# Kernel optimization log

Hardware: AMD Instinct MI355X
Metric: run time of the kernel (lower is better)

## Reference

```python
import jax, jax.numpy as jnp
import numpy as np

DIM, K_RANK, L, N_CLASS = 64, 16, 8, 10
H = 1e-3
B = 256
DD = DIM * DIM  # 4096


def _cay(C, D):
    # Cayley transform of B = C @ D^T : I + C (I - 0.5 D^T C)^{-1} D^T
    Id = jnp.eye(C.shape[1], dtype=C.dtype)
    DT = jnp.swapaxes(D, 1, 2)
    inv = jnp.linalg.inv(Id - 0.5 * DT @ C)
    return Id + C @ inv @ DT


def setup_inputs() -> dict:
    key = jax.random.key(0)
    ks = jax.random.split(key, 9)
    u = jax.random.normal(ks[0], (B, DIM, K_RANK), jnp.float32) / np.float32(np.sqrt(DIM))
    vh = jax.random.normal(ks[1], (B, K_RANK, DIM), jnp.float32) / np.float32(np.sqrt(DIM))
    eye_k = jnp.eye(K_RANK, dtype=jnp.float32)
    off = 0.05 * jax.random.normal(ks[2], (B, K_RANK, K_RANK), jnp.float32) * (1.0 - eye_k)
    dvals = jax.random.uniform(ks[3], (B, K_RANK), jnp.float32, 0.5, 1.5)
    s_core = off + dvals[:, :, None] * eye_k  # diag bounded away from 0 (invert_S)
    s_block = jnp.zeros((B, DIM, K_RANK), jnp.float32).at[:, :K_RANK, :K_RANK].set(s_core)
    X = jnp.stack([u.reshape(B, -1), s_block.reshape(B, -1), vh.reshape(B, -1)], axis=1)
    sc = np.float32(1.0 / np.sqrt(DD))
    W0 = sc * jax.random.normal(ks[4], (DD, DD), jnp.float32)
    W = sc * jax.random.normal(ks[5], (L, DD, DD), jnp.float32)
    b = sc * jax.random.normal(ks[6], (L, DD), jnp.float32)
    Wc = sc * jax.random.normal(ks[7], (N_CLASS, DD), jnp.float32)
    bc = sc * jax.random.normal(ks[8], (N_CLASS,), jnp.float32)
    return {"X": X, "W0": W0, "W": W, "b": b, "Wc": Wc, "bc": bc}


def reference(X, W0, W, b, Wc, bc):
    Bn = X.shape[0]
    u = X[:, 0].reshape(Bn, DIM, K_RANK)
    s = X[:, 1].reshape(Bn, DIM, K_RANK)[:, :K_RANK, :K_RANK]
    vh = X[:, 2].reshape(Bn, K_RANK, DIM)
    v = jnp.swapaxes(vh, 1, 2)
    eye_k = jnp.eye(K_RANK, dtype=X.dtype)
    eye_d = jnp.eye(DIM, dtype=X.dtype)
    Xf = (u @ s @ vh).reshape(Bn, DD)
    outs = []
    for i in range(L + 1):  # layer 0 has no bias
        lin = Xf @ W0.T if i == 0 else Xf @ W[i - 1].T + b[i - 1]
        dY = jax.nn.relu(lin).reshape(Bn, DIM, DIM)
        # invert_S: invert only the diagonal of s
        s_inv = (1.0 / jnp.diagonal(s, axis1=1, axis2=2))[:, :, None] * eye_k
        dU = dY @ v @ s_inv
        dV = jnp.swapaxes(dY, 1, 2) @ u @ jnp.swapaxes(s_inv, 1, 2)
        dS = jnp.swapaxes(u, 1, 2) @ dY @ v
        uT = jnp.swapaxes(u, 1, 2)
        F = (eye_d - u @ uT) @ dU
        FT = jnp.swapaxes(F, 1, 2)
        u = _cay(H * (F @ uT), -H * (u @ FT)) @ u
        vT = jnp.swapaxes(v, 1, 2)
        F = (eye_d - v @ vT) @ dV
        FT = jnp.swapaxes(F, 1, 2)
        v = _cay(H * (F @ vT), -H * (v @ FT)) @ v
        s = s + H * dS
        Xf = (u @ s @ jnp.swapaxes(v, 1, 2)).reshape(Bn, DD)
        outs.append(Xf)
    X_transformed = jnp.stack(outs, axis=-1)  # (B, dim*dim, L+1)
    X_classified = Xf @ Wc.T + bc
    X_predicted = jax.nn.softmax(X_classified, axis=1)
    return X_predicted, X_classified, X_transformed
```

## Files before the change

### kernel.cpp

```cpp
#include <hip/hip_runtime.h>
#include <hip/hip_cooperative_groups.h>
#include <math.h>

namespace cg = cooperative_groups;

typedef unsigned short u16;
typedef unsigned int u32;
using bf16x8 = __attribute__((ext_vector_type(8))) short;
using f32x4  = __attribute__((ext_vector_type(4))) float;

#define DD 4096
#define NB 256
#define SPLIT_K 8
#define PSTRIDE (NB * DD)
#define PLANE (NB * DD)

__device__ __forceinline__ u16 f2bf(float f) {
  unsigned int u = __float_as_uint(f);
  u += 0x7fffu + ((u >> 16) & 1u);
  return (u16)(u >> 16);
}
__device__ __forceinline__ float bf2f(u16 h) {
  return __uint_as_float((u32)h << 16);
}
__device__ __forceinline__ unsigned int pack2bf(float a, float b) {
  return (unsigned int)f2bf(a) | ((unsigned int)f2bf(b) << 16);
}
__device__ __forceinline__ void async_cp16(const u16* g, u16* l) {
  __builtin_amdgcn_global_load_lds(
      (const __attribute__((address_space(1))) unsigned int*)g,
      (__attribute__((address_space(3))) unsigned int*)l, 16, 0, 0);
}

struct GemmSmem {
  u16 As[256 * 64];
  u16 Bs[64 * 64];
};
struct UpdSmem {
  float U[64][17], V[64][17], P[64][17], Q[64][17];
  float S[16][16];
  float sinv[16];
  union {
    float dY[64][68];
    struct {
      float F[64][17];
      float T1[16][17], G1[16][17], G2[16][17], M1[16][17], dSs[16][17];
      float RS[512];
    };
  };
};
struct PackSmem { float buf[512 * 9]; };
struct ClsSmem  { float red[8][10]; };

__device__ __forceinline__ void gemm_phase(
    GemmSmem& sm, const u16* __restrict__ A, const float* __restrict__ W,
    u16* __restrict__ part, int tile, int t)
{
  const int nt = tile & 63, kz = tile >> 6;
  const int w = t >> 6, l = t & 63;
  const int colg0 = nt << 6;
  const int k0 = kz << 9;

  f32x4 acc[4][2];
#pragma unroll
  for (int mi = 0; mi < 4; ++mi)
#pragma unroll
    for (int nj = 0; nj < 2; ++nj)
      acc[mi][nj] = (f32x4){0.f, 0.f, 0.f, 0.f};

  const int wm = w & 3, wn = w >> 2;
  const int lr = l & 15, lg = l >> 4;
  const int arow_l = (w << 3) + (l >> 3);
  const int acl = l & 7;
  const int bn_l = t >> 3;
  const int bcc = t & 7;

  for (int tt = 0; tt < 8; ++tt) {
    const int kk = k0 + (tt << 6);
    __syncthreads();
#pragma unroll
    for (int r = 0; r < 4; ++r) {
      const int row = (r << 6) + arow_l;
      const int cs = acl ^ (row & 7);
      async_cp16(A + ((size_t)row << 12) + kk + (cs << 3),
                 &sm.As[(r << 12) + (w << 9)]);
    }
    {
      const float* wsrc = W + ((size_t)(colg0 + bn_l) << 12) + kk + (bcc << 3);
      const float4 f0 = *reinterpret_cast<const float4*>(wsrc);
      const float4 f1 = *reinterpret_cast<const float4*>(wsrc + 4);
      uint4 pk;
      pk.x = pack2bf(f0.x, f0.y);
      pk.y = pack2bf(f0.z, f0.w);
      pk.z = pack2bf(f1.x, f1.y);
      pk.w = pack2bf(f1.z, f1.w);
      *reinterpret_cast<uint4*>(&sm.Bs[(bn_l << 6) + ((bcc ^ (bn_l & 7)) << 3)]) = pk;
    }
    __syncthreads();
#pragma unroll
    for (int ks = 0; ks < 2; ++ks) {
      const int cg2 = (ks << 2) + lg;
      bf16x8 av[4], bv[2];
#pragma unroll
      for (int mi = 0; mi < 4; ++mi) {
        const int fr = (wm << 6) + (mi << 4) + lr;
        av[mi] = *reinterpret_cast<const bf16x8*>(&sm.As[(fr << 6) + ((cg2 ^ (fr & 7)) << 3)]);
      }
#pragma unroll
      for (int nj = 0; nj < 2; ++nj) {
        const int fc = (wn << 5) + (nj << 4) + lr;
        bv[nj] = *reinterpret_cast<const bf16x8*>(&sm.Bs[(fc << 6) + ((cg2 ^ (fc & 7)) << 3)]);
      }
#pragma unroll
      for (int mi = 0; mi < 4; ++mi)
#pragma unroll
        for (int nj = 0; nj < 2; ++nj)
          acc[mi][nj] = __builtin_amdgcn_mfma_f32_16x16x32_bf16(
              av[mi], bv[nj], acc[mi][nj], 0, 0, 0);
    }
  }

  u16* pout = part + (size_t)kz * PSTRIDE;
#pragma unroll
  for (int mi = 0; mi < 4; ++mi)
#pragma unroll
    for (int nj = 0; nj < 2; ++nj) {
      const int col = colg0 + (wn << 5) + (nj << 4) + lr;
#pragma unroll
      for (int j = 0; j < 4; ++j) {
        const int row = (wm << 6) + (mi << 4) + (lg << 2) + j;
        pout[((size_t)row << 12) + col] = f2bf(acc[mi][nj][j]);
      }
    }
}

__device__ __forceinline__ void stiefel_update512(
    UpdSmem& m, float (&Am)[64][17], float (&Dm)[64][17],
    int t, float* __restrict__ gout, size_t ub)
{
  const int p = t >> 3;
  const int j0 = (t << 1) & 15;
  {
    const int half = t & 1, i = t >> 5, j = (t >> 1) & 15;
    float a = 0.f;
    const int r0 = half << 5;
    for (int r = r0; r < r0 + 32; ++r) a += Am[r][i] * Dm[r][j];
    m.RS[t] = a;
  }
  __syncthreads();
  if (t < 256) m.T1[t >> 4][t & 15] = m.RS[t << 1] + m.RS[(t << 1) + 1];
  __syncthreads();
  {
    float f0 = Dm[p][j0], f1 = Dm[p][j0 + 1];
    for (int k = 0; k < 16; ++k) {
      const float ak = Am[p][k];
      f0 -= ak * m.T1[k][j0];
      f1 -= ak * m.T1[k][j0 + 1];
    }
    m.F[p][j0] = f0; m.F[p][j0 + 1] = f1;
  }
  __syncthreads();
  if (t < 256) {
    const int i = t >> 4, j = t & 15;
    float g = 0.f;
    for (int r = 0; r < 64; ++r) g += Am[r][i] * m.F[r][j];
    m.G1[i][j] = g;
  } else {
    const int tt = t - 256, i = tt >> 4, j = tt & 15;
    float g = 0.f;
    for (int r = 0; r < 64; ++r) g += Am[r][i] * Am[r][j];
    m.G2[i][j] = g;
  }
  __syncthreads();
  if (t < 256) {
    const int i = t >> 4, j = t & 15;
    float mm = 0.f;
    for (int k = 0; k < 16; ++k) mm += m.G1[i][k] * m.G2[k][j];
    m.M1[i][j] = mm;
  }
  __syncthreads();
  {
    float a0 = 0.f, a1 = 0.f;
    for (int k = 0; k < 16; ++k) {
      const float fk = m.F[p][k];
      a0 += fk * m.M1[k][j0];
      a1 += fk * m.M1[k][j0 + 1];
    }
    const float n0 = Am[p][j0] - 1e-6f * a0;
    const float n1 = Am[p][j0 + 1] - 1e-6f * a1;
    __syncthreads();
    Am[p][j0] = n0; Am[p][j0 + 1] = n1;
    *reinterpret_cast<float2*>(gout + ub + (p << 4) + j0) = make_float2(n0, n1);
  }
  __syncthreads();
}

__device__ __forceinline__ void write_xf_tail(
    UpdSmem& m, int t, int b, float* __restrict__ Xf, u16* __restrict__ Xfb,
    float* __restrict__ outL_plane)
{
  const int p = t >> 3;
  const int j0 = (t << 1) & 15;
  {
    float a0 = 0.f, a1 = 0.f;
    for (int k = 0; k < 16; ++k) {
      const float uk = m.U[p][k];
      a0 += uk * m.S[k][j0];
      a1 += uk * m.S[k][j0 + 1];
    }
    m.P[p][j0] = a0; m.P[p][j0 + 1] = a1;
  }
  __syncthreads();
  {
    const int q0 = (t & 7) << 3;
    float res[8];
#pragma unroll
    for (int e = 0; e < 8; ++e) res[e] = 0.f;
    for (int i = 0; i < 16; ++i) {
      const float pi = m.P[p][i];
#pragma unroll
      for (int e = 0; e < 8; ++e) res[e] += pi * m.V[q0 + e][i];
    }
    const size_t ko = ((size_t)b << 12) + (p << 6) + q0;
    float4* xo = reinterpret_cast<float4*>(Xf + ko);
    const float4 r0 = make_float4(res[0], res[1], res[2], res[3]);
    const float4 r1 = make_float4(res[4], res[5], res[6], res[7]);
    xo[0] = r0; xo[1] = r1;
    uint4 pk;
    pk.x = pack2bf(res[0], res[1]); pk.y = pack2bf(res[2], res[3]);
    pk.z = pack2bf(res[4], res[5]); pk.w = pack2bf(res[6], res[7]);
    *reinterpret_cast<uint4*>(Xfb + ko) = pk;
    if (outL_plane != nullptr) {
      float4* op = reinterpret_cast<float4*>(outL_plane + ko);
      op[0] = r0; op[1] = r1;
    }
  }
}

__device__ __forceinline__ void update_phase(
    UpdSmem& m, const u16* __restrict__ part, const float* __restrict__ bias,
    float* __restrict__ u_g, float* __restrict__ v_g, float* __restrict__ s_g,
    float* __restrict__ Xf, u16* __restrict__ Xfb,
    float* __restrict__ outL_plane, int b, int t)
{
  const size_t ub = (size_t)b << 10;
  {
    const float2 u2 = *reinterpret_cast<const float2*>(u_g + ub + (t << 1));
    const float2 v2 = *reinterpret_cast<const float2*>(v_g + ub + (t << 1));
    const int r = t >> 3, c = (t & 7) << 1;
    m.U[r][c] = u2.x; m.U[r][c + 1] = u2.y;
    m.V[r][c] = v2.x; m.V[r][c + 1] = v2.y;
    if (t < 256) m.S[t >> 4][t & 15] = s_g[((size_t)b << 8) + t];
  }
  __syncthreads();
  if (t < 16) m.sinv[t] = 1.0f / m.S[t][t];
  {
    const u16* p0 = part + ((size_t)b << 12) + (t << 3);
    float x[8];
#pragma unroll
    for (int e = 0; e < 8; ++e) x[e] = 0.f;
#pragma unroll
    for (int kzi = 0; kzi < SPLIT_K; ++kzi) {
      const uint4 v = *reinterpret_cast<const uint4*>(p0 + (size_t)kzi * PSTRIDE);
      x[0] += bf2f((u16)(v.x & 0xffff)); x[1] += bf2f((u16)(v.x >> 16));
      x[2] += bf2f((u16)(v.y & 0xffff)); x[3] += bf2f((u16)(v.y >> 16));
      x[4] += bf2f((u16)(v.z & 0xffff)); x[5] += bf2f((u16)(v.z >> 16));
      x[6] += bf2f((u16)(v.w & 0xffff)); x[7] += bf2f((u16)(v.w >> 16));
    }
    if (bias != nullptr) {
      const float4 b0 = *reinterpret_cast<const float4*>(bias + (t << 3));
      const float4 b1 = *reinterpret_cast<const float4*>(bias + (t << 3) + 4);
      x[0] += b0.x; x[1] += b0.y; x[2] += b0.z; x[3] += b0.w;
      x[4] += b1.x; x[5] += b1.y; x[6] += b1.z; x[7] += b1.w;
    }
    const int r = t >> 3, c = (t & 7) << 3;
    float4* d0 = reinterpret_cast<float4*>(&m.dY[r][c]);
    d0[0] = make_float4(fmaxf(x[0], 0.f), fmaxf(x[1], 0.f), fmaxf(x[2], 0.f), fmaxf(x[3], 0.f));
    d0[1] = make_float4(fmaxf(x[4], 0.f), fmaxf(x[5], 0.f), fmaxf(x[6], 0.f), fmaxf(x[7], 0.f));
  }
  __syncthreads();
  const int p = t >> 3;
  const int j0 = (t << 1) & 15;
  {
    float a0 = 0.f, a1 = 0.f;
    for (int q = 0; q < 64; ++q) {
      const float d = m.dY[p][q];
      a0 += d * m.V[q][j0];
      a1 += d * m.V[q][j0 + 1];
    }
    float b0 = 0.f, b1 = 0.f;
    for (int r = 0; r < 64; ++r) {
      const float d = m.dY[r][p];
      b0 += d * m.U[r][j0];
      b1 += d * m.U[r][j0 + 1];
    }
    m.P[p][j0] = a0; m.P[p][j0 + 1] = a1;
    m.Q[p][j0] = b0; m.Q[p][j0 + 1] = b1;
  }
  __syncthreads();
  {
    const int half = t & 1, i = t >> 5, j = (t >> 1) & 15;
    float a = 0.f;
    const int r0 = half << 5;
    for (int r = r0; r < r0 + 32; ++r) a += m.U[r][i] * m.P[r][j];
    m.RS[t] = a;
  }
  __syncthreads();
  if (t < 256) m.dSs[t >> 4][t & 15] = m.RS[t << 1] + m.RS[(t << 1) + 1];
  __syncthreads();
  for (int i = t; i < 1024; i += 512) {
    const int r = i >> 4, c = i & 15;
    const float sc = m.sinv[c];
    m.P[r][c] *= sc;
    m.Q[r][c] *= sc;
  }
  __syncthreads();

  stiefel_update512(m, m.U, m.P, t, u_g, ub);
  stiefel_update512(m, m.V, m.Q, t, v_g, ub);

  if (t < 256) {
    const int i = t >> 4, j = t & 15;
    const float ns = m.S[i][j] + 1e-3f * m.dSs[i][j];
    m.S[i][j] = ns;
    s_g[((size_t)b << 8) + t] = ns;
  }
  __syncthreads();
  write_xf_tail(m, t, b, Xf, Xfb, outL_plane);
}

__device__ __forceinline__ void init_phase(
    UpdSmem& m, const float* __restrict__ X,
    float* __restrict__ u_g, float* __restrict__ v_g, float* __restrict__ s_g,
    float* __restrict__ Xf, u16* __restrict__ Xfb, int b, int t)
{
  const float* xb = X + (size_t)b * 3072;
  const size_t ub = (size_t)b << 10;
  {
    const float2 u2 = *reinterpret_cast<const float2*>(xb + (t << 1));
    const int r = t >> 3, c = (t & 7) << 1;
    m.U[r][c] = u2.x; m.U[r][c + 1] = u2.y;
    *reinterpret_cast<float2*>(u_g + ub + (t << 1)) = u2;
    if (t < 256) {
      const float sv = xb[1024 + t];
      m.S[t >> 4][t & 15] = sv;
      s_g[((size_t)b << 8) + t] = sv;
    }
    const float2 v2 = *reinterpret_cast<const float2*>(xb + 2048 + (t << 1));
    const int g2 = t << 1;
    const int iv = g2 >> 6, q = g2 & 63;
    m.V[q][iv] = v2.x; m.V[q + 1][iv] = v2.y;
    v_g[ub + (size_t)q * 16 + iv] = v2.x;
    v_g[ub + (size_t)(q + 1) * 16 + iv] = v2.y;
  }
  __syncthreads();
  write_xf_tail(m, t, b, Xf, Xfb, nullptr);
}

__global__ __launch_bounds__(512, 4) void mega_kernel(
    const float* __restrict__ X, const float* __restrict__ W0,
    const float* __restrict__ W, const float* __restrict__ bb,
    const float* __restrict__ Wc, const float* __restrict__ bc,
    float* __restrict__ pred, float* __restrict__ cls, float* __restrict__ outT,
    float* __restrict__ Xf, u16* __restrict__ part,
    float* __restrict__ u_g, float* __restrict__ v_g, float* __restrict__ s_g,
    u16* __restrict__ Xfb, float* __restrict__ outL)
{
  cg::grid_group grid = cg::this_grid();
  __shared__ __align__(16) char smem_raw[sizeof(GemmSmem)];
  GemmSmem& gs = *reinterpret_cast<GemmSmem*>(smem_raw);
  UpdSmem&  us = *reinterpret_cast<UpdSmem*>(smem_raw);
  PackSmem& ps = *reinterpret_cast<PackSmem*>(smem_raw);
  ClsSmem&  cs = *reinterpret_cast<ClsSmem*>(smem_raw);

  const int g = blockIdx.x, t = threadIdx.x;
  const int nwg = gridDim.x;

  for (int b = g; b < NB; b += nwg)
    init_phase(us, X, u_g, v_g, s_g, Xf, Xfb, b, t);
  grid.sync();

  for (int layer = 0; layer <= 8; ++layer) {
    const float* Wl = (layer == 0) ? W0 : W + (size_t)(layer - 1) * DD * DD;
    for (int tile = g; tile < 64 * SPLIT_K; tile += nwg)
      gemm_phase(gs, Xfb, Wl, part, tile, t);
    grid.sync();
    for (int b = g; b < NB; b += nwg)
      update_phase(us, part, (layer == 0) ? nullptr : (bb + (size_t)(layer - 1) * DD),
                   u_g, v_g, s_g, Xf, Xfb,
                   outL + (size_t)layer * PLANE, b, t);
    grid.sync();
  }

  for (int b = g; b < NB; b += nwg) {
    const int lane = t & 63, w = t >> 6;
    float acc[10];
#pragma unroll
    for (int c = 0; c < 10; ++c) acc[c] = 0.f;
    const float* xr = Xf + ((size_t)b << 12);
    for (int k = t; k < 4096; k += 512) {
      const float x = xr[k];
#pragma unroll
      for (int c = 0; c < 10; ++c) acc[c] += x * Wc[c * 4096 + k];
    }
#pragma unroll
    for (int c = 0; c < 10; ++c)
      for (int off = 32; off; off >>= 1) acc[c] += __shfl_xor(acc[c], off);
    if (lane == 0)
#pragma unroll
      for (int c = 0; c < 10; ++c) cs.red[w][c] = acc[c];
    __syncthreads();
    if (t == 0) {
      float lg[10], ex[10];
      float mx = -1e30f;
#pragma unroll
      for (int c = 0; c < 10; ++c) {
        float s8 = 0.f;
#pragma unroll
        for (int ww = 0; ww < 8; ++ww) s8 += cs.red[ww][c];
        lg[c] = s8 + bc[c];
        mx = fmaxf(mx, lg[c]);
      }
      float s = 0.f;
#pragma unroll
      for (int c = 0; c < 10; ++c) { ex[c] = expf(lg[c] - mx); s += ex[c]; }
      const float inv = 1.f / s;
#pragma unroll
      for (int c = 0; c < 10; ++c) {
        cls[b * 10 + c] = lg[c];
        pred[b * 10 + c] = ex[c] * inv;
      }
    }
    __syncthreads();
  }

  for (int ch = g; ch < 2048; ch += nwg) {
    const int base = ch << 9;
#pragma unroll
    for (int l = 0; l < 9; ++l)
      ps.buf[t * 9 + l] = outL[(size_t)l * PLANE + base + t];
    __syncthreads();
    const float4* b4 = reinterpret_cast<const float4*>(ps.buf);
    float4* o4 = reinterpret_cast<float4*>(outT + (size_t)base * 9);
    for (int i = t; i < 1152; i += 512) o4[i] = b4[i];
    __syncthreads();
  }
}

__global__ __launch_bounds__(512, 4) void gemm_kernel(
    const u16* __restrict__ A, const float* __restrict__ W,
    u16* __restrict__ part)
{
  __shared__ __align__(16) GemmSmem sm;
  gemm_phase(sm, A, W, part, (int)(blockIdx.x + (blockIdx.y << 6)), (int)threadIdx.x);
}

__global__ __launch_bounds__(512) void update_kernel(
    const u16* __restrict__ part, const float* __restrict__ bias,
    float* __restrict__ u_g, float* __restrict__ v_g, float* __restrict__ s_g,
    float* __restrict__ Xf, u16* __restrict__ Xfb,
    float* __restrict__ outL, int layer)
{
  __shared__ __align__(16) UpdSmem m;
  update_phase(m, part, bias, u_g, v_g, s_g, Xf, Xfb,
               outL + (size_t)layer * PLANE, (int)blockIdx.x, (int)threadIdx.x);
}

__global__ __launch_bounds__(512) void init_kernel(
    const float* __restrict__ X, float* __restrict__ u_g, float* __restrict__ v_g,
    float* __restrict__ s_g, float* __restrict__ Xf, u16* __restrict__ Xfb)
{
  __shared__ __align__(16) UpdSmem m;
  init_phase(m, X, u_g, v_g, s_g, Xf, Xfb, (int)blockIdx.x, (int)threadIdx.x);
}

__global__ __launch_bounds__(256) void pack_kernel(
    const float* __restrict__ outL, float* __restrict__ outT)
{
  const int t = threadIdx.x;
  const int base = blockIdx.x << 8;
  __shared__ float buf[256 * 9];
#pragma unroll
  for (int l = 0; l < 9; ++l)
    buf[t * 9 + l] = outL[(size_t)l * PLANE + base + t];
  __syncthreads();
  const float4* b4 = reinterpret_cast<const float4*>(buf);
  float4* o4 = reinterpret_cast<float4*>(outT + (size_t)base * 9);
  for (int i = t; i < 576; i += 256) o4[i] = b4[i];
}

__global__ __launch_bounds__(256) void classifier_kernel(
    const float* __restrict__ Xf, const float* __restrict__ Wc,
    const float* __restrict__ bc, float* __restrict__ pred, float* __restrict__ cls)
{
  const int b = blockIdx.x, t = threadIdx.x;
  const int lane = t & 63, w = t >> 6;
  __shared__ float red[4][10];
  float acc[10];
#pragma unroll
  for (int c = 0; c < 10; ++c) acc[c] = 0.f;
  const float* xr = Xf + ((size_t)b << 12);
  for (int k = t; k < 4096; k += 256) {
    const float x = xr[k];
#pragma unroll
    for (int c = 0; c < 10; ++c) acc[c] += x * Wc[c * 4096 + k];
  }
#pragma unroll
  for (int c = 0; c < 10; ++c)
    for (int off = 32; off; off >>= 1) acc[c] += __shfl_xor(acc[c], off);
  if (lane == 0)
#pragma unroll
    for (int c = 0; c < 10; ++c) red[w][c] = acc[c];
  __syncthreads();
  if (t == 0) {
    float lg[10], ex[10];
    float m = -1e30f;
#pragma unroll
    for (int c = 0; c < 10; ++c) {
      lg[c] = red[0][c] + red[1][c] + red[2][c] + red[3][c] + bc[c];
      m = fmaxf(m, lg[c]);
    }
    float s = 0.f;
#pragma unroll
    for (int c = 0; c < 10; ++c) { ex[c] = expf(lg[c] - m); s += ex[c]; }
    const float inv = 1.f / s;
#pragma unroll
    for (int c = 0; c < 10; ++c) {
      cls[b * 10 + c] = lg[c];
      pred[b * 10 + c] = ex[c] * inv;
    }
  }
}

extern "C" void kernel_launch(void* const* d_in, const int* in_sizes, int n_in,
                              void* d_out, int out_size, void* d_ws, size_t ws_size,
                              hipStream_t stream) {
  (void)in_sizes; (void)n_in; (void)out_size; (void)ws_size;
  const float* X  = (const float*)d_in[0];
  const float* W0 = (const float*)d_in[1];
  const float* W  = (const float*)d_in[2];
  const float* bb = (const float*)d_in[3];
  const float* Wc = (const float*)d_in[4];
  const float* bc = (const float*)d_in[5];

  float* out_pred  = (float*)d_out;
  float* out_cls   = out_pred + 2560;
  float* out_trans = out_pred + 5120;

  char* ws = (char*)d_ws;
  float* Xf   = (float*)(ws);
  u16*   part = (u16*)  (ws + (4ull << 20));
  float* u_g  = (float*)(ws + (20ull << 20));
  float* v_g  = (float*)(ws + (21ull << 20));
  float* s_g  = (float*)(ws + (22ull << 20));
  u16*   Xfb  = (u16*)  (ws + (23ull << 20));
  float* outL = (float*)(ws + (25ull << 20));

  int occ = 0;
  (void)hipOccupancyMaxActiveBlocksPerMultiprocessor(
      &occ, (const void*)mega_kernel, 512, 0);

  bool done = false;
  if (occ >= 2) {
    void* kargs[] = {
      (void*)&X, (void*)&W0, (void*)&W, (void*)&bb, (void*)&Wc, (void*)&bc,
      (void*)&out_pred, (void*)&out_cls, (void*)&out_trans,
      (void*)&Xf, (void*)&part, (void*)&u_g, (void*)&v_g, (void*)&s_g,
      (void*)&Xfb, (void*)&outL
    };
    hipError_t e = hipLaunchCooperativeKernel((const void*)mega_kernel,
                                              dim3(512), dim3(512),
                                              kargs, 0, stream);
    if (e == hipSuccess) done = true;
    else (void)hipGetLastError();
  }

  if (!done) {
    init_kernel<<<NB, 512, 0, stream>>>(X, u_g, v_g, s_g, Xf, Xfb);
    for (int i = 0; i <= 8; ++i) {
      const float* Wl = (i == 0) ? W0 : W + (size_t)(i - 1) * DD * DD;
      gemm_kernel<<<dim3(64, SPLIT_K), 512, 0, stream>>>(Xfb, Wl, part);
      update_kernel<<<NB, 512, 0, stream>>>(
          part, (i == 0) ? nullptr : (bb + (size_t)(i - 1) * DD),
          u_g, v_g, s_g, Xf, Xfb, outL, i);
    }
    pack_kernel<<<4096, 256, 0, stream>>>(outL, out_trans);
    classifier_kernel<<<NB, 256, 0, stream>>>(Xf, Wc, bc, out_pred, out_cls);
  }
}
```

Baseline: 436.5 us.

## Double-buffer GEMM LDS tiles and prefetch next K-slice during MFMA

```diff
diff --git a/kernel.cpp b/kernel.cpp
--- a/kernel.cpp
+++ b/kernel.cpp
@@ -33,8 +33,8 @@
 }
 
 struct GemmSmem {
-  u16 As[256 * 64];
-  u16 Bs[64 * 64];
+  u16 As[2][256 * 64];
+  u16 Bs[2][64 * 64];
 };
 struct UpdSmem {
   float U[64][17], V[64][17], P[64][17], Q[64][17];
@@ -75,28 +75,47 @@
   const int bn_l = t >> 3;
   const int bcc = t & 7;
 
+  float4 b0[2], b1[2];
+
+#define ISSUE_A(tt) do {                                                     \
+    const int kkk = k0 + ((tt) << 6);                                        \
+    _Pragma("unroll")                                                        \
+    for (int r = 0; r < 4; ++r) {                                            \
+      const int row = (r << 6) + arow_l;                                     \
+      const int cs = acl ^ (row & 7);                                        \
+      async_cp16(A + ((size_t)row << 12) + kkk + (cs << 3),                  \
+                 &sm.As[(tt) & 1][(r << 12) + (w << 9)]);                    \
+    } } while (0)
+
+#define LOAD_B(tt) do {                                                      \
+    const float* wsrc = W + ((size_t)(colg0 + bn_l) << 12) + k0 +            \
+                        ((tt) << 6) + (bcc << 3);                            \
+    b0[(tt) & 1] = *reinterpret_cast<const float4*>(wsrc);                   \
+    b1[(tt) & 1] = *reinterpret_cast<const float4*>(wsrc + 4);               \
+  } while (0)
+
+  ISSUE_A(0); LOAD_B(0);
+  __builtin_amdgcn_sched_barrier(0);
+
+#pragma unroll
   for (int tt = 0; tt < 8; ++tt) {
-    const int kk = k0 + (tt << 6);
-    __syncthreads();
-#pragma unroll
-    for (int r = 0; r < 4; ++r) {
-      const int row = (r << 6) + arow_l;
-      const int cs = acl ^ (row & 7);
-      async_cp16(A + ((size_t)row << 12) + kk + (cs << 3),
-                 &sm.As[(r << 12) + (w << 9)]);
-    }
+    const int pb = tt & 1;
+    if (tt < 7) { ISSUE_A(tt + 1); LOAD_B(tt + 1); }
+    __builtin_amdgcn_sched_barrier(0);
+    if (tt < 7) { asm volatile("s_waitcnt vmcnt(6)" ::: "memory"); }
+    else        { asm volatile("s_waitcnt vmcnt(0)" ::: "memory"); }
+    __builtin_amdgcn_sched_barrier(0);
     {
-      const float* wsrc = W + ((size_t)(colg0 + bn_l) << 12) + kk + (bcc << 3);
-      const float4 f0 = *reinterpret_cast<const float4*>(wsrc);
-      const float4 f1 = *reinterpret_cast<const float4*>(wsrc + 4);
       uint4 pk;
-      pk.x = pack2bf(f0.x, f0.y);
-      pk.y = pack2bf(f0.z, f0.w);
-      pk.z = pack2bf(f1.x, f1.y);
-      pk.w = pack2bf(f1.z, f1.w);
-      *reinterpret_cast<uint4*>(&sm.Bs[(bn_l << 6) + ((bcc ^ (bn_l & 7)) << 3)]) = pk;
-    }
-    __syncthreads();
+      pk.x = pack2bf(b0[pb].x, b0[pb].y);
+      pk.y = pack2bf(b0[pb].z, b0[pb].w);
+      pk.z = pack2bf(b1[pb].x, b1[pb].y);
+      pk.w = pack2bf(b1[pb].z, b1[pb].w);
+      *reinterpret_cast<uint4*>(&sm.Bs[pb][(bn_l << 6) + ((bcc ^ (bn_l & 7)) << 3)]) = pk;
+    }
+    asm volatile("s_waitcnt lgkmcnt(0)" ::: "memory");
+    __builtin_amdgcn_s_barrier();
+    __builtin_amdgcn_sched_barrier(0);
 #pragma unroll
     for (int ks = 0; ks < 2; ++ks) {
       const int cg2 = (ks << 2) + lg;
@@ -104,12 +123,12 @@
 #pragma unroll
       for (int mi = 0; mi < 4; ++mi) {
         const int fr = (wm << 6) + (mi << 4) + lr;
-        av[mi] = *reinterpret_cast<const bf16x8*>(&sm.As[(fr << 6) + ((cg2 ^ (fr & 7)) << 3)]);
+        av[mi] = *reinterpret_cast<const bf16x8*>(&sm.As[pb][(fr << 6) + ((cg2 ^ (fr & 7)) << 3)]);
       }
 #pragma unroll
       for (int nj = 0; nj < 2; ++nj) {
         const int fc = (wn << 5) + (nj << 4) + lr;
-        bv[nj] = *reinterpret_cast<const bf16x8*>(&sm.Bs[(fc << 6) + ((cg2 ^ (fc & 7)) << 3)]);
+        bv[nj] = *reinterpret_cast<const bf16x8*>(&sm.Bs[pb][(fc << 6) + ((cg2 ^ (fc & 7)) << 3)]);
       }
 #pragma unroll
       for (int mi = 0; mi < 4; ++mi)
@@ -118,7 +137,10 @@
           acc[mi][nj] = __builtin_amdgcn_mfma_f32_16x16x32_bf16(
               av[mi], bv[nj], acc[mi][nj], 0, 0, 0);
     }
-  }
+    __builtin_amdgcn_s_barrier();
+  }
+#undef ISSUE_A
+#undef LOAD_B
 
   u16* pout = part + (size_t)kz * PSTRIDE;
 #pragma unroll
```

Measured after the change: 441.3 us. About the same (+1.1%).

## Replace cooperative mega-kernel with per-layer launches and double split-K

Applied to the files above, without the earlier changes.

```diff
diff --git a/kernel.cpp b/kernel.cpp
--- a/kernel.cpp
+++ b/kernel.cpp
@@ -1,8 +1,5 @@
 #include <hip/hip_runtime.h>
-#include <hip/hip_cooperative_groups.h>
 #include <math.h>
-
-namespace cg = cooperative_groups;
 
 typedef unsigned short u16;
 typedef unsigned int u32;
@@ -11,7 +8,7 @@
 
 #define DD 4096
 #define NB 256
-#define SPLIT_K 8
+#define SPLIT_K 16
 #define PSTRIDE (NB * DD)
 #define PLANE (NB * DD)
 
@@ -32,10 +29,94 @@
       (__attribute__((address_space(3))) unsigned int*)l, 16, 0, 0);
 }
 
-struct GemmSmem {
-  u16 As[256 * 64];
-  u16 Bs[64 * 64];
-};
+__global__ __launch_bounds__(512, 8) void gemm_kernel(
+    const u16* __restrict__ A, const float* __restrict__ W,
+    u16* __restrict__ part)
+{
+  const int nt = blockIdx.x;
+  const int kz = blockIdx.y;
+  const int t = threadIdx.x;
+  const int w = t >> 6, l = t & 63;
+
+  __shared__ __align__(16) u16 As[256 * 64];
+  __shared__ __align__(16) u16 Bs[64 * 64];
+
+  const int colg0 = nt << 6;
+  const int k0 = kz << 8;
+
+  f32x4 acc[4][2];
+#pragma unroll
+  for (int mi = 0; mi < 4; ++mi)
+#pragma unroll
+    for (int nj = 0; nj < 2; ++nj)
+      acc[mi][nj] = (f32x4){0.f, 0.f, 0.f, 0.f};
+
+  const int wm = w & 3, wn = w >> 2;
+  const int lr = l & 15, lg = l >> 4;
+  const int arow_l = (w << 3) + (l >> 3);
+  const int acl = l & 7;
+  const int bn_l = t >> 3;
+  const int bcc = t & 7;
+
+  for (int tt = 0; tt < 4; ++tt) {
+    const int kk = k0 + (tt << 6);
+    __syncthreads();
+#pragma unroll
+    for (int r = 0; r < 4; ++r) {
+      const int row = (r << 6) + arow_l;
+      const int cs = acl ^ (row & 7);
+      async_cp16(A + ((size_t)row << 12) + kk + (cs << 3),
+                 &As[(r << 12) + (w << 9)]);
+    }
+    {
+      const float* wsrc = W + ((size_t)(colg0 + bn_l) << 12) + kk + (bcc << 3);
+      const float4 f0 = *reinterpret_cast<const float4*>(wsrc);
+      const float4 f1 = *reinterpret_cast<const float4*>(wsrc + 4);
+      uint4 pk;
+      pk.x = pack2bf(f0.x, f0.y);
+      pk.y = pack2bf(f0.z, f0.w);
+      pk.z = pack2bf(f1.x, f1.y);
+      pk.w = pack2bf(f1.z, f1.w);
+      *reinterpret_cast<uint4*>(&Bs[(bn_l << 6) + ((bcc ^ (bn_l & 7)) << 3)]) = pk;
+    }
+    __syncthreads();
+#pragma unroll
+    for (int ks = 0; ks < 2; ++ks) {
+      const int cg = (ks << 2) + lg;
+      bf16x8 av[4], bv[2];
+#pragma unroll
+      for (int mi = 0; mi < 4; ++mi) {
+        const int fr = (wm << 6) + (mi << 4) + lr;
+        av[mi] = *reinterpret_cast<const bf16x8*>(&As[(fr << 6) + ((cg ^ (fr & 7)) << 3)]);
+      }
+#pragma unroll
+      for (int nj = 0; nj < 2; ++nj) {
+        const int fc = (wn << 5) + (nj << 4) + lr;
+        bv[nj] = *reinterpret_cast<const bf16x8*>(&Bs[(fc << 6) + ((cg ^ (fc & 7)) << 3)]);
+      }
+#pragma unroll
+      for (int mi = 0; mi < 4; ++mi)
+#pragma unroll
+        for (int nj = 0; nj < 2; ++nj)
+          acc[mi][nj] = __builtin_amdgcn_mfma_f32_16x16x32_bf16(
+              av[mi], bv[nj], acc[mi][nj], 0, 0, 0);
+    }
+  }
+
+  u16* pout = part + (size_t)kz * PSTRIDE;
+#pragma unroll
+  for (int mi = 0; mi < 4; ++mi)
+#pragma unroll
+    for (int nj = 0; nj < 2; ++nj) {
+      const int col = colg0 + (wn << 5) + (nj << 4) + lr;
+#pragma unroll
+      for (int j = 0; j < 4; ++j) {
+        const int row = (wm << 6) + (mi << 4) + (lg << 2) + j;
+        pout[((size_t)row << 12) + col] = f2bf(acc[mi][nj][j]);
+      }
+    }
+}
+
 struct UpdSmem {
   float U[64][17], V[64][17], P[64][17], Q[64][17];
   float S[16][16];
@@ -49,90 +130,6 @@
     };
   };
 };
-struct PackSmem { float buf[512 * 9]; };
-struct ClsSmem  { float red[8][10]; };
-
-__device__ __forceinline__ void gemm_phase(
-    GemmSmem& sm, const u16* __restrict__ A, const float* __restrict__ W,
-    u16* __restrict__ part, int tile, int t)
-{
-  const int nt = tile & 63, kz = tile >> 6;
-  const int w = t >> 6, l = t & 63;
-  const int colg0 = nt << 6;
-  const int k0 = kz << 9;
-
-  f32x4 acc[4][2];
-#pragma unroll
-  for (int mi = 0; mi < 4; ++mi)
-#pragma unroll
-    for (int nj = 0; nj < 2; ++nj)
-      acc[mi][nj] = (f32x4){0.f, 0.f, 0.f, 0.f};
-
-  const int wm = w & 3, wn = w >> 2;
-  const int lr = l & 15, lg = l >> 4;
-  const int arow_l = (w << 3) + (l >> 3);
-  const int acl = l & 7;
-  const int bn_l = t >> 3;
-  const int bcc = t & 7;
-
-  for (int tt = 0; tt < 8; ++tt) {
-    const int kk = k0 + (tt << 6);
-    __syncthreads();
-#pragma unroll
-    for (int r = 0; r < 4; ++r) {
-      const int row = (r << 6) + arow_l;
-      const int cs = acl ^ (row & 7);
-      async_cp16(A + ((size_t)row << 12) + kk + (cs << 3),
-                 &sm.As[(r << 12) + (w << 9)]);
-    }
-    {
-      const float* wsrc = W + ((size_t)(colg0 + bn_l) << 12) + kk + (bcc << 3);
-      const float4 f0 = *reinterpret_cast<const float4*>(wsrc);
-      const float4 f1 = *reinterpret_cast<const float4*>(wsrc + 4);
-      uint4 pk;
-      pk.x = pack2bf(f0.x, f0.y);
-      pk.y = pack2bf(f0.z, f0.w);
-      pk.z = pack2bf(f1.x, f1.y);
-      pk.w = pack2bf(f1.z, f1.w);
-      *reinterpret_cast<uint4*>(&sm.Bs[(bn_l << 6) + ((bcc ^ (bn_l & 7)) << 3)]) = pk;
-    }
-    __syncthreads();
-#pragma unroll
-    for (int ks = 0; ks < 2; ++ks) {
-      const int cg2 = (ks << 2) + lg;
-      bf16x8 av[4], bv[2];
-#pragma unroll
-      for (int mi = 0; mi < 4; ++mi) {
-        const int fr = (wm << 6) + (mi << 4) + lr;
-        av[mi] = *reinterpret_cast<const bf16x8*>(&sm.As[(fr << 6) + ((cg2 ^ (fr & 7)) << 3)]);
-      }
-#pragma unroll
-      for (int nj = 0; nj < 2; ++nj) {
-        const int fc = (wn << 5) + (nj << 4) + lr;
-        bv[nj] = *reinterpret_cast<const bf16x8*>(&sm.Bs[(fc << 6) + ((cg2 ^ (fc & 7)) << 3)]);
-      }
-#pragma unroll
-      for (int mi = 0; mi < 4; ++mi)
-#pragma unroll
-        for (int nj = 0; nj < 2; ++nj)
-          acc[mi][nj] = __builtin_amdgcn_mfma_f32_16x16x32_bf16(
-              av[mi], bv[nj], acc[mi][nj], 0, 0, 0);
-    }
-  }
-
-  u16* pout = part + (size_t)kz * PSTRIDE;
-#pragma unroll
-  for (int mi = 0; mi < 4; ++mi)
-#pragma unroll
-    for (int nj = 0; nj < 2; ++nj) {
-      const int col = colg0 + (wn << 5) + (nj << 4) + lr;
-#pragma unroll
-      for (int j = 0; j < 4; ++j) {
-        const int row = (wm << 6) + (mi << 4) + (lg << 2) + j;
-        pout[((size_t)row << 12) + col] = f2bf(acc[mi][nj][j]);
-      }
-    }
-}
 
 __device__ __forceinline__ void stiefel_update512(
     UpdSmem& m, float (&Am)[64][17], float (&Dm)[64][17],
@@ -237,12 +234,16 @@
   }
 }
 
-__device__ __forceinline__ void update_phase(
-    UpdSmem& m, const u16* __restrict__ part, const float* __restrict__ bias,
+__global__ __launch_bounds__(512) void update_kernel(
+    const u16* __restrict__ part, const float* __restrict__ bias,
     float* __restrict__ u_g, float* __restrict__ v_g, float* __restrict__ s_g,
     float* __restrict__ Xf, u16* __restrict__ Xfb,
-    float* __restrict__ outL_plane, int b, int t)
-{
+    float* __restrict__ outL, int layer)
+{
+  const int b = blockIdx.x, t = threadIdx.x;
+  __shared__ __align__(16) UpdSmem m;
+  float* outL_plane = outL + (size_t)layer * PLANE;
+
   const size_t ub = (size_t)b << 10;
   {
     const float2 u2 = *reinterpret_cast<const float2*>(u_g + ub + (t << 1));
@@ -329,11 +330,12 @@
   write_xf_tail(m, t, b, Xf, Xfb, outL_plane);
 }
 
-__device__ __forceinline__ void init_phase(
-    UpdSmem& m, const float* __restrict__ X,
-    float* __restrict__ u_g, float* __restrict__ v_g, float* __restrict__ s_g,
-    float* __restrict__ Xf, u16* __restrict__ Xfb, int b, int t)
-{
+__global__ __launch_bounds__(512) void init_kernel(
+    const float* __restrict__ X, float* __restrict__ u_g, float* __restrict__ v_g,
+    float* __restrict__ s_g, float* __restrict__ Xf, u16* __restrict__ Xfb)
+{
+  const int b = blockIdx.x, t = threadIdx.x;
+  __shared__ __align__(16) UpdSmem m;
   const float* xb = X + (size_t)b * 3072;
   const size_t ub = (size_t)b << 10;
   {
@@ -355,123 +357,6 @@
   }
   __syncthreads();
   write_xf_tail(m, t, b, Xf, Xfb, nullptr);
-}
-
-__global__ __launch_bounds__(512, 4) void mega_kernel(
-    const float* __restrict__ X, const float* __restrict__ W0,
-    const float* __restrict__ W, const float* __restrict__ bb,
-    const float* __restrict__ Wc, const float* __restrict__ bc,
-    float* __restrict__ pred, float* __restrict__ cls, float* __restrict__ outT,
-    float* __restrict__ Xf, u16* __restrict__ part,
-    float* __restrict__ u_g, float* __restrict__ v_g, float* __restrict__ s_g,
-    u16* __restrict__ Xfb, float* __restrict__ outL)
-{
-  cg::grid_group grid = cg::this_grid();
-  __shared__ __align__(16) char smem_raw[sizeof(GemmSmem)];
-  GemmSmem& gs = *reinterpret_cast<GemmSmem*>(smem_raw);
-  UpdSmem&  us = *reinterpret_cast<UpdSmem*>(smem_raw);
-  PackSmem& ps = *reinterpret_cast<PackSmem*>(smem_raw);
-  ClsSmem&  cs = *reinterpret_cast<ClsSmem*>(smem_raw);
-
-  const int g = blockIdx.x, t = threadIdx.x;
-  const int nwg = gridDim.x;
-
-  for (int b = g; b < NB; b += nwg)
-    init_phase(us, X, u_g, v_g, s_g, Xf, Xfb, b, t);
-  grid.sync();
-
-  for (int layer = 0; layer <= 8; ++layer) {
-    const float* Wl = (layer == 0) ? W0 : W + (size_t)(layer - 1) * DD * DD;
-    for (int tile = g; tile < 64 * SPLIT_K; tile += nwg)
-      gemm_phase(gs, Xfb, Wl, part, tile, t);
-    grid.sync();
-    for (int b = g; b < NB; b += nwg)
-      update_phase(us, part, (layer == 0) ? nullptr : (bb + (size_t)(layer - 1) * DD),
-                   u_g, v_g, s_g, Xf, Xfb,
-                   outL + (size_t)layer * PLANE, b, t);
-    grid.sync();
-  }
-
-  for (int b = g; b < NB; b += nwg) {
-    const int lane = t & 63, w = t >> 6;
-    float acc[10];
-#pragma unroll
-    for (int c = 0; c < 10; ++c) acc[c] = 0.f;
-    const float* xr = Xf + ((size_t)b << 12);
-    for (int k = t; k < 4096; k += 512) {
-      const float x = xr[k];
-#pragma unroll
-      for (int c = 0; c < 10; ++c) acc[c] += x * Wc[c * 4096 + k];
-    }
-#pragma unroll
-    for (int c = 0; c < 10; ++c)
-      for (int off = 32; off; off >>= 1) acc[c] += __shfl_xor(acc[c], off);
-    if (lane == 0)
-#pragma unroll
-      for (int c = 0; c < 10; ++c) cs.red[w][c] = acc[c];
-    __syncthreads();
-    if (t == 0) {
-      float lg[10], ex[10];
-      float mx = -1e30f;
-#pragma unroll
-      for (int c = 0; c < 10; ++c) {
-        float s8 = 0.f;
-#pragma unroll
-        for (int ww = 0; ww < 8; ++ww) s8 += cs.red[ww][c];
-        lg[c] = s8 + bc[c];
-        mx = fmaxf(mx, lg[c]);
-      }
-      float s = 0.f;
-#pragma unroll
-      for (int c = 0; c < 10; ++c) { ex[c] = expf(lg[c] - mx); s += ex[c]; }
-      const float inv = 1.f / s;
-#pragma unroll
-      for (int c = 0; c < 10; ++c) {
-        cls[b * 10 + c] = lg[c];
-        pred[b * 10 + c] = ex[c] * inv;
-      }
-    }
-    __syncthreads();
-  }
-
-  for (int ch = g; ch < 2048; ch += nwg) {
-    const int base = ch << 9;
-#pragma unroll
-    for (int l = 0; l < 9; ++l)
-      ps.buf[t * 9 + l] = outL[(size_t)l * PLANE + base + t];
-    __syncthreads();
-    const float4* b4 = reinterpret_cast<const float4*>(ps.buf);
-    float4* o4 = reinterpret_cast<float4*>(outT + (size_t)base * 9);
-    for (int i = t; i < 1152; i += 512) o4[i] = b4[i];
-    __syncthreads();
-  }
-}
-
-__global__ __launch_bounds__(512, 4) void gemm_kernel(
-    const u16* __restrict__ A, const float* __restrict__ W,
-    u16* __restrict__ part)
-{
-  __shared__ __align__(16) GemmSmem sm;
-  gemm_phase(sm, A, W, part, (int)(blockIdx.x + (blockIdx.y << 6)), (int)threadIdx.x);
-}
-
-__global__ __launch_bounds__(512) void update_kernel(
-    const u16* __restrict__ part, const float* __restrict__ bias,
-    float* __restrict__ u_g, float* __restrict__ v_g, float* __restrict__ s_g,
-    float* __restrict__ Xf, u16* __restrict__ Xfb,
-    float* __restrict__ outL, int layer)
-{
-  __shared__ __align__(16) UpdSmem m;
-  update_phase(m, part, bias, u_g, v_g, s_g, Xf, Xfb,
-               outL + (size_t)layer * PLANE, (int)blockIdx.x, (int)threadIdx.x);
-}
-
-__global__ __launch_bounds__(512) void init_kernel(
-    const float* __restrict__ X, float* __restrict__ u_g, float* __restrict__ v_g,
-    float* __restrict__ s_g, float* __restrict__ Xf, u16* __restrict__ Xfb)
-{
-  __shared__ __align__(16) UpdSmem m;
-  init_phase(m, X, u_g, v_g, s_g, Xf, Xfb, (int)blockIdx.x, (int)threadIdx.x);
 }
 
 __global__ __launch_bounds__(256) void pack_kernel(
@@ -550,41 +435,20 @@
   char* ws = (char*)d_ws;
   float* Xf   = (float*)(ws);
   u16*   part = (u16*)  (ws + (4ull << 20));
-  float* u_g  = (float*)(ws + (20ull << 20));
-  float* v_g  = (float*)(ws + (21ull << 20));
-  float* s_g  = (float*)(ws + (22ull << 20));
-  u16*   Xfb  = (u16*)  (ws + (23ull << 20));
-  float* outL = (float*)(ws + (25ull << 20));
-
-  int occ = 0;
-  (void)hipOccupancyMaxActiveBlocksPerMultiprocessor(
-      &occ, (const void*)mega_kernel, 512, 0);
-
-  bool done = false;
-  if (occ >= 2) {
-    void* kargs[] = {
-      (void*)&X, (void*)&W0, (void*)&W, (void*)&bb, (void*)&Wc, (void*)&bc,
-      (void*)&out_pred, (void*)&out_cls, (void*)&out_trans,
-      (void*)&Xf, (void*)&part, (void*)&u_g, (void*)&v_g, (void*)&s_g,
-      (void*)&Xfb, (void*)&outL
-    };
-    hipError_t e = hipLaunchCooperativeKernel((const void*)mega_kernel,
-                                              dim3(512), dim3(512),
-                                              kargs, 0, stream);
-    if (e == hipSuccess) done = true;
-    else (void)hipGetLastError();
-  }
-
-  if (!done) {
-    init_kernel<<<NB, 512, 0, stream>>>(X, u_g, v_g, s_g, Xf, Xfb);
-    for (int i = 0; i <= 8; ++i) {
-      const float* Wl = (i == 0) ? W0 : W + (size_t)(i - 1) * DD * DD;
-      gemm_kernel<<<dim3(64, SPLIT_K), 512, 0, stream>>>(Xfb, Wl, part);
-      update_kernel<<<NB, 512, 0, stream>>>(
-          part, (i == 0) ? nullptr : (bb + (size_t)(i - 1) * DD),
-          u_g, v_g, s_g, Xf, Xfb, outL, i);
-    }
-    pack_kernel<<<4096, 256, 0, stream>>>(outL, out_trans);
-    classifier_kernel<<<NB, 256, 0, stream>>>(Xf, Wc, bc, out_pred, out_cls);
-  }
-}
+  float* u_g  = (float*)(ws + (36ull << 20));
+  float* v_g  = (float*)(ws + (37ull << 20));
+  float* s_g  = (float*)(ws + (38ull << 20));
+  u16*   Xfb  = (u16*)  (ws + (39ull << 20));
+  float* outL = (float*)(ws + (41ull << 20));
+
+  init_kernel<<<NB, 512, 0, stream>>>(X, u_g, v_g, s_g, Xf, Xfb);
+  for (int i = 0; i <= 8; ++i) {
+    const float* Wl = (i == 0) ? W0 : W + (size_t)(i - 1) * DD * DD;
+    gemm_kernel<<<dim3(64, SPLIT_K), 512, 0, stream>>>(Xfb, Wl, part);
+    update_kernel<<<NB, 512, 0, stream>>>(
+        part, (i == 0) ? nullptr : (bb + (size_t)(i - 1) * DD),
+        u_g, v_g, s_g, Xf, Xfb, outL, i);
+  }
+  pack_kernel<<<4096, 256, 0, stream>>>(outL, out_trans);
+  classifier_kernel<<<NB, 256, 0, stream>>>(Xf, Wc, bc, out_pred, out_cls);
+}
```

Measured after the change: 655.9 us. +50.3%, slower.
